# Kernel tuning notes

Hardware: AMD Instinct MI355X
Metric: run time of the kernel (lower is better)

## Reference

```python
import jax, jax.numpy as jnp
import numpy as np

TEMPERATURE = 10.0
EPS = 1e-12  # torch F.normalize eps


def setup_inputs() -> dict:
    key = jax.random.key(0)
    k1, k2 = jax.random.split(key)
    B, D = 8192, 1024
    text_embeddings = jax.random.normal(k1, (B, D), dtype=jnp.float32)
    image_embeddings = jax.random.normal(k2, (B, D), dtype=jnp.float32)
    bias = jnp.zeros((1,), dtype=jnp.float32)
    return {
        "text_embeddings": text_embeddings,
        "image_embeddings": image_embeddings,
        "bias": bias,
    }


def _normalize(x):
    # matches torch F.normalize(p=2, dim=1): x / max(||x||, eps)
    norm = jnp.linalg.norm(x, axis=-1, keepdims=True)
    return x / jnp.maximum(norm, EPS)


def reference(text_embeddings, image_embeddings, bias):
    B = text_embeddings.shape[0]
    img_n = _normalize(image_embeddings)   # [B, D]
    txt_n = _normalize(text_embeddings)    # [B, D]
    # similarity[i, j] = <img_i, txt_j>
    sim = jnp.einsum('id,jd->ij', img_n, txt_n)          # [B, B]
    logits = sim * (-TEMPERATURE) + bias[0]
    labels = 2.0 * jnp.eye(B, dtype=logits.dtype) - 1.0   # +1 diag, -1 off-diag
    # loss_ij = log(1/(1+exp(label*logit))) = -softplus(label*logit)
    total_loss = -jnp.sum(jax.nn.softplus(labels * logits))
    return -(total_loss / B)
```

## Files before the change

kernel.cpp:

```cpp
#include <hip/hip_runtime.h>
#include <stdint.h>
#include <stddef.h>

#define NROWS 8192
#define DIM   1024
#define TEMP  10.0f

#define BM 256
#define BN 128
#define BK 128

typedef __attribute__((ext_vector_type(8))) int i32x8;
typedef __attribute__((ext_vector_type(4))) float floatx4;

__device__ __forceinline__ void load16_lds(const unsigned char* g, unsigned char* l) {
    __builtin_amdgcn_global_load_lds(
        (__attribute__((address_space(1))) void*)(g),
        (__attribute__((address_space(3))) void*)(l),
        16, 0, 0);
}

__device__ __forceinline__ i32x8 pack8(int4 lo, int4 hi) {
    i32x8 r;
    r[0] = lo.x; r[1] = lo.y; r[2] = lo.z; r[3] = lo.w;
    r[4] = hi.x; r[5] = hi.y; r[6] = hi.z; r[7] = hi.w;
    return r;
}

__global__ __launch_bounds__(256) void normalize_kernel(
    const float* __restrict__ img, const float* __restrict__ txt,
    unsigned char* __restrict__ imgq, unsigned char* __restrict__ txtq,
    float* __restrict__ out)
{
    const int gw = blockIdx.x * 4 + (threadIdx.x >> 6);
    const int lane = threadIdx.x & 63;
    const float* src;
    unsigned char* dst;
    if (gw < NROWS) {
        src = img + (size_t)gw * DIM;
        dst = imgq + (size_t)gw * DIM;
    } else {
        src = txt + (size_t)(gw - NROWS) * DIM;
        dst = txtq + (size_t)(gw - NROWS) * DIM;
    }
    float4 v[4];
    float ss = 0.f;
#pragma unroll
    for (int c = 0; c < 4; c++) {
        v[c] = ((const float4*)src)[lane * 4 + c];
        ss += v[c].x * v[c].x + v[c].y * v[c].y + v[c].z * v[c].z + v[c].w * v[c].w;
    }
#pragma unroll
    for (int off = 32; off; off >>= 1) ss += __shfl_xor(ss, off);
    const float scale = 1.0f / fmaxf(sqrtf(ss), 1e-12f);
    int4 o;
    int* op = (int*)&o;
#pragma unroll
    for (int c = 0; c < 4; c++) {
        int p = 0;
        p = __builtin_amdgcn_cvt_pk_fp8_f32(v[c].x * scale, v[c].y * scale, p, false);
        p = __builtin_amdgcn_cvt_pk_fp8_f32(v[c].z * scale, v[c].w * scale, p, true);
        op[c] = p;
    }
    ((int4*)dst)[lane] = o;
    if (gw == 0 && lane == 0) out[0] = 0.f;
}

__global__ __launch_bounds__(256, 2) void simloss_kernel(
    const unsigned char* __restrict__ An,
    const unsigned char* __restrict__ Bn,
    const float* __restrict__ bias,
    float* __restrict__ out)
{
    __shared__ unsigned char As[BM * BK];
    __shared__ unsigned char Bs[2][BN * BK];
    __shared__ float red[12];

    const int t = threadIdx.x;
    const int lane = t & 63;
    const int wave = t >> 6;

    const int bid = blockIdx.x;
    const int blockN = (bid & 7) + 8 * ((bid >> 3) & 7);
    const int blockM = bid >> 6;

    const int srow = t >> 3;
    const int g = (t & 7) ^ ((t >> 3) & 7);
    const unsigned char* gA = An + (size_t)(blockM * BM + srow) * DIM + g * 16;
    const unsigned char* gB = Bn + (size_t)(blockN * BN + srow) * DIM + g * 16;
    unsigned char* lA = &As[t * 16];

    const int waveM = (wave >> 1) * 128;
    const int waveN = (wave & 1) * 64;
    const int fr = lane & 15;
    const int fq = lane >> 4;
    const int o0 = ((2 * fq) ^ (fr & 7)) * 16;

    floatx4 acc[8][4];
#pragma unroll
    for (int mi = 0; mi < 8; mi++)
#pragma unroll
        for (int ni = 0; ni < 4; ni++)
            acc[mi][ni] = (floatx4){0.f, 0.f, 0.f, 0.f};

#pragma unroll
    for (int c = 0; c < 4; c++)
        load16_lds(gB + (size_t)c * 32 * DIM, &Bs[0][t * 16 + c * 4096]);

#pragma unroll
    for (int it = 0; it < DIM / BK; it++) {
        const int k0 = it * BK;
        const int cur = it & 1;
        __syncthreads();
#pragma unroll
        for (int c = 0; c < 8; c++)
            load16_lds(gA + (size_t)c * 32 * DIM + k0, lA + c * 4096);
        if (it < DIM / BK - 1) {
#pragma unroll
            for (int c = 0; c < 4; c++)
                load16_lds(gB + (size_t)c * 32 * DIM + k0 + BK,
                           &Bs[cur ^ 1][t * 16 + c * 4096]);
            asm volatile("s_waitcnt vmcnt(4)" ::: "memory");
        } else {
            asm volatile("s_waitcnt vmcnt(0)" ::: "memory");
        }
        __syncthreads();

        asm volatile("s_setprio 1");
        i32x8 b[4];
#pragma unroll
        for (int ni = 0; ni < 4; ni++) {
            const int row = waveN + ni * 16 + fr;
            b[ni] = pack8(*(const int4*)&Bs[cur][row * BK + o0],
                          *(const int4*)&Bs[cur][row * BK + (o0 ^ 16)]);
        }
#pragma unroll
        for (int mi = 0; mi < 8; mi++) {
            const int row = waveM + mi * 16 + fr;
            i32x8 a = pack8(*(const int4*)&As[row * BK + o0],
                            *(const int4*)&As[row * BK + (o0 ^ 16)]);
#pragma unroll
            for (int ni = 0; ni < 4; ni++)
                acc[mi][ni] = __builtin_amdgcn_mfma_scale_f32_16x16x128_f8f6f4(
                    a, b[ni], acc[mi][ni],
                    0, 0,
                    0, 0x7f7f7f7f,
                    0, 0x7f7f7f7f);
        }
        asm volatile("s_setprio 0");
    }

    const float bv = bias[0];
    const float c1 = -TEMP * 1.4426950408889634f;
    const float c0 = bv * 1.4426950408889634f;
    float accP = 0.f, accQ = 0.f, accD = 0.f;
    const int gi0 = blockM * BM + waveM + fq * 4;
    const int gj0 = blockN * BN + waveN + fr;
#pragma unroll
    for (int mi = 0; mi < 8; mi++) {
#pragma unroll
        for (int ni = 0; ni < 4; ni++) {
#pragma unroll
            for (int r = 0; r < 4; r++) {
                float s = acc[mi][ni][r];
                float w = fmaf(s, c1, c0);
                float e2 = __builtin_amdgcn_exp2f(-fabsf(w));
                accP += __builtin_amdgcn_logf(1.0f + e2);
                accP = fmaf(0.5f, fabsf(w), accP);
                accQ += s;
            }
        }
    }
    const bool diagblk = ((blockN >> 1) == blockM);
    if (diagblk) {
#pragma unroll
        for (int mi = 0; mi < 8; mi++)
#pragma unroll
            for (int ni = 0; ni < 4; ni++)
#pragma unroll
                for (int r = 0; r < 4; r++) {
                    int ig = gi0 + mi * 16 + r;
                    int jg = gj0 + ni * 16;
                    if (ig == jg) accD += acc[mi][ni][r];
                }
    }
#pragma unroll
    for (int off = 32; off; off >>= 1) {
        accP += __shfl_xor(accP, off);
        accQ += __shfl_xor(accQ, off);
        accD += __shfl_xor(accD, off);
    }
    if (lane == 0) {
        red[wave * 3 + 0] = accP;
        red[wave * 3 + 1] = accQ;
        red[wave * 3 + 2] = accD;
    }
    __syncthreads();
    if (t == 0) {
        float P = red[0] + red[3] + red[6] + red[9];
        float Q = red[1] + red[4] + red[7] + red[10];
        float D = red[2] + red[5] + red[8] + red[11];
        float contrib = fmaf(0.6931471805599453f, P, fmaf(5.0f, Q, -16384.0f * bv));
        if (diagblk) contrib += fmaf(-TEMP, D, 128.0f * bv);
        atomicAdd(out, contrib * (1.0f / 8192.0f));
    }
}

extern "C" void kernel_launch(void* const* d_in, const int* in_sizes, int n_in,
                              void* d_out, int out_size, void* d_ws, size_t ws_size,
                              hipStream_t stream) {
    const float* txt = (const float*)d_in[0];
    const float* img = (const float*)d_in[1];
    const float* bias = (const float*)d_in[2];
    float* out = (float*)d_out;

    unsigned char* imgq = (unsigned char*)d_ws;
    unsigned char* txtq = imgq + (size_t)NROWS * DIM;

    normalize_kernel<<<dim3(2 * NROWS / 4), dim3(256), 0, stream>>>(
        img, txt, imgq, txtq, out);

    simloss_kernel<<<dim3((NROWS / BM) * (NROWS / BN)), dim3(256), 0, stream>>>(
        imgq, txtq, bias, out);
}
```

Baseline: 168.6 us.

## Switch GEMM to 32x32x64 FP8 MFMA tiles with per-k-step fragment loads

Replaces the 16x16x128 scaled FP8 MFMA with the 32x32x64 variant, which reorganizes each wave's 128x64 tile into 4x2 fragments, splits each BK block into two k-steps, and remaps the epilogue's diagonal indexing to the 32x32 output layout. The larger MFMA shape is meant to cut LDS fragment reads per flop and raise matrix-core efficiency. The normalize kernel also changes to a strided per-lane float4 load and 4-byte stores for coalescing. The accumulator register count is unchanged, but the LDS swizzle interaction and instruction scheduling differ.

Result: faster. 162.6 us (-3.5%).

```diff
diff --git a/kernel.cpp b/kernel.cpp
--- a/kernel.cpp
+++ b/kernel.cpp
@@ -11,7 +11,7 @@
 #define BK 128
 
 typedef __attribute__((ext_vector_type(8))) int i32x8;
-typedef __attribute__((ext_vector_type(4))) float floatx4;
+typedef __attribute__((ext_vector_type(16))) float floatx16;
 
 __device__ __forceinline__ void load16_lds(const unsigned char* g, unsigned char* l) {
     __builtin_amdgcn_global_load_lds(
@@ -20,11 +20,12 @@
         16, 0, 0);
 }
 
-__device__ __forceinline__ i32x8 pack8(int4 lo, int4 hi) {
-    i32x8 r;
-    r[0] = lo.x; r[1] = lo.y; r[2] = lo.z; r[3] = lo.w;
-    r[4] = hi.x; r[5] = hi.y; r[6] = hi.z; r[7] = hi.w;
-    return r;
+__device__ __forceinline__ i32x8 ldfrag(const unsigned char* rowbase, int r7, int kb4) {
+    const int o0 = (kb4 ^ r7) << 4;
+    union { i32x8 v; int4 q[2]; } u;
+    u.q[0] = *(const int4*)(rowbase + o0);
+    u.q[1] = *(const int4*)(rowbase + (o0 ^ 16));
+    return u.v;
 }
 
 __global__ __launch_bounds__(256) void normalize_kernel(
@@ -47,22 +48,19 @@
     float ss = 0.f;
 #pragma unroll
     for (int c = 0; c < 4; c++) {
-        v[c] = ((const float4*)src)[lane * 4 + c];
+        v[c] = ((const float4*)src)[lane + 64 * c];
         ss += v[c].x * v[c].x + v[c].y * v[c].y + v[c].z * v[c].z + v[c].w * v[c].w;
     }
 #pragma unroll
     for (int off = 32; off; off >>= 1) ss += __shfl_xor(ss, off);
     const float scale = 1.0f / fmaxf(sqrtf(ss), 1e-12f);
-    int4 o;
-    int* op = (int*)&o;
 #pragma unroll
     for (int c = 0; c < 4; c++) {
         int p = 0;
         p = __builtin_amdgcn_cvt_pk_fp8_f32(v[c].x * scale, v[c].y * scale, p, false);
         p = __builtin_amdgcn_cvt_pk_fp8_f32(v[c].z * scale, v[c].w * scale, p, true);
-        op[c] = p;
-    }
-    ((int4*)dst)[lane] = o;
+        ((int*)dst)[lane + 64 * c] = p;
+    }
     if (gw == 0 && lane == 0) out[0] = 0.f;
 }
 
@@ -92,16 +90,31 @@
 
     const int waveM = (wave >> 1) * 128;
     const int waveN = (wave & 1) * 64;
-    const int fr = lane & 15;
-    const int fq = lane >> 4;
-    const int o0 = ((2 * fq) ^ (fr & 7)) * 16;
-
-    floatx4 acc[8][4];
-#pragma unroll
-    for (int mi = 0; mi < 8; mi++)
-#pragma unroll
-        for (int ni = 0; ni < 4; ni++)
-            acc[mi][ni] = (floatx4){0.f, 0.f, 0.f, 0.f};
+    const int fr = lane & 31;
+    const int fh = lane >> 5;
+
+    const unsigned char* arow[4];
+    const unsigned char* brow0[2];
+    int ar7[4], br7[2];
+#pragma unroll
+    for (int mi = 0; mi < 4; mi++) {
+        const int r = waveM + mi * 32 + fr;
+        arow[mi] = &As[r * BK];
+        ar7[mi] = r & 7;
+    }
+#pragma unroll
+    for (int ni = 0; ni < 2; ni++) {
+        const int r = waveN + ni * 32 + fr;
+        brow0[ni] = &Bs[0][r * BK];
+        br7[ni] = r & 7;
+    }
+
+    floatx16 acc[4][2];
+#pragma unroll
+    for (int mi = 0; mi < 4; mi++)
+#pragma unroll
+        for (int ni = 0; ni < 2; ni++)
+            acc[mi][ni] = (floatx16)(0.f);
 
 #pragma unroll
     for (int c = 0; c < 4; c++)
@@ -127,25 +140,25 @@
         __syncthreads();
 
         asm volatile("s_setprio 1");
-        i32x8 b[4];
-#pragma unroll
-        for (int ni = 0; ni < 4; ni++) {
-            const int row = waveN + ni * 16 + fr;
-            b[ni] = pack8(*(const int4*)&Bs[cur][row * BK + o0],
-                          *(const int4*)&Bs[cur][row * BK + (o0 ^ 16)]);
-        }
-#pragma unroll
-        for (int mi = 0; mi < 8; mi++) {
-            const int row = waveM + mi * 16 + fr;
-            i32x8 a = pack8(*(const int4*)&As[row * BK + o0],
-                            *(const int4*)&As[row * BK + (o0 ^ 16)]);
-#pragma unroll
-            for (int ni = 0; ni < 4; ni++)
-                acc[mi][ni] = __builtin_amdgcn_mfma_scale_f32_16x16x128_f8f6f4(
-                    a, b[ni], acc[mi][ni],
-                    0, 0,
-                    0, 0x7f7f7f7f,
-                    0, 0x7f7f7f7f);
+        const int boff = cur * (BN * BK);
+#pragma unroll
+        for (int ks = 0; ks < 2; ks++) {
+            const int kb4 = ks * 4 + fh * 2;
+            i32x8 b[2];
+#pragma unroll
+            for (int ni = 0; ni < 2; ni++)
+                b[ni] = ldfrag(brow0[ni] + boff, br7[ni], kb4);
+#pragma unroll
+            for (int mi = 0; mi < 4; mi++) {
+                i32x8 a = ldfrag(arow[mi], ar7[mi], kb4);
+#pragma unroll
+                for (int ni = 0; ni < 2; ni++)
+                    acc[mi][ni] = __builtin_amdgcn_mfma_scale_f32_32x32x64_f8f6f4(
+                        a, b[ni], acc[mi][ni],
+                        0, 0,
+                        0, 0x7f7f7f7f,
+                        0, 0x7f7f7f7f);
+            }
         }
         asm volatile("s_setprio 0");
     }
@@ -154,15 +167,15 @@
     const float c1 = -TEMP * 1.4426950408889634f;
     const float c0 = bv * 1.4426950408889634f;
     float accP = 0.f, accQ = 0.f, accD = 0.f;
-    const int gi0 = blockM * BM + waveM + fq * 4;
+    const int gi0 = blockM * BM + waveM + 4 * fh;
     const int gj0 = blockN * BN + waveN + fr;
 #pragma unroll
-    for (int mi = 0; mi < 8; mi++) {
-#pragma unroll
-        for (int ni = 0; ni < 4; ni++) {
-#pragma unroll
-            for (int r = 0; r < 4; r++) {
-                float s = acc[mi][ni][r];
+    for (int mi = 0; mi < 4; mi++) {
+#pragma unroll
+        for (int ni = 0; ni < 2; ni++) {
+#pragma unroll
+            for (int reg = 0; reg < 16; reg++) {
+                float s = acc[mi][ni][reg];
                 float w = fmaf(s, c1, c0);
                 float e2 = __builtin_amdgcn_exp2f(-fabsf(w));
                 accP += __builtin_amdgcn_logf(1.0f + e2);
@@ -174,14 +187,14 @@
     const bool diagblk = ((blockN >> 1) == blockM);
     if (diagblk) {
 #pragma unroll
-        for (int mi = 0; mi < 8; mi++)
-#pragma unroll
-            for (int ni = 0; ni < 4; ni++)
-#pragma unroll
-                for (int r = 0; r < 4; r++) {
-                    int ig = gi0 + mi * 16 + r;
-                    int jg = gj0 + ni * 16;
-                    if (ig == jg) accD += acc[mi][ni][r];
+        for (int mi = 0; mi < 4; mi++)
+#pragma unroll
+            for (int ni = 0; ni < 2; ni++)
+#pragma unroll
+                for (int reg = 0; reg < 16; reg++) {
+                    int ig = gi0 + mi * 32 + (reg & 3) + 8 * (reg >> 2);
+                    int jg = gj0 + ni * 32;
+                    if (ig == jg) accD += acc[mi][ni][reg];
                 }
     }
 #pragma unroll
```
